# Performance work log

Hardware: AMD Instinct MI355X
Metric: run time of the kernel (lower is better)

## Reference

```python
import jax, jax.numpy as jnp
import numpy as np

FEAT_RES = 512
FEAT_DIM = 48
WIDTH = 128
IN_DIM = FEAT_DIM + 27 + 63  # 138
N_RAYS, N_SAMPLES = 4096, 128


def positional_encode(x, L):
    freqs = (2.0 ** jnp.arange(L)).astype(x.dtype)            # [L]
    xf = x[..., None, :] * freqs[:, None]                      # [..., L, 3]
    enc = jnp.concatenate([jnp.sin(xf), jnp.cos(xf)], axis=-1) # [..., L, 6]
    return jnp.concatenate([x, enc.reshape(x.shape[:-1] + (L * 6,))], axis=-1)


def grid_sample_bilinear(plane, gx, gy):
    # plane: [C, H, W]; gx, gy: [N, S] in [-1, 1]; align_corners=True, zeros padding
    H, W = plane.shape[-2], plane.shape[-1]
    ix = (gx + 1.0) * 0.5 * (W - 1)
    iy = (gy + 1.0) * 0.5 * (H - 1)
    x0 = jnp.floor(ix); y0 = jnp.floor(iy)
    x1 = x0 + 1.0;      y1 = y0 + 1.0
    wx1 = ix - x0; wx0 = 1.0 - wx1
    wy1 = iy - y0; wy0 = 1.0 - wy1

    def gather(xi, yi, w):
        valid = (xi >= 0) & (xi <= W - 1) & (yi >= 0) & (yi <= H - 1)
        xc = jnp.clip(xi, 0, W - 1).astype(jnp.int32)
        yc = jnp.clip(yi, 0, H - 1).astype(jnp.int32)
        v = plane[:, yc, xc]                                   # [C, N, S]
        return v * (w * valid.astype(w.dtype))[None]

    return (gather(x0, y0, wx0 * wy0) + gather(x1, y0, wx1 * wy0)
            + gather(x0, y1, wx0 * wy1) + gather(x1, y1, wx1 * wy1))


def setup_inputs() -> dict:
    key = jax.random.key(0)
    ks = jax.random.split(key, 12)
    x = jax.random.uniform(ks[0], (N_RAYS, N_SAMPLES, 3), jnp.float32, -3.0, 3.0)
    d = jax.random.normal(ks[1], (N_RAYS, 3), jnp.float32)
    d = d / jnp.linalg.norm(d, axis=-1, keepdims=True)
    feat = jax.random.normal(ks[2], (3, FEAT_DIM, FEAT_RES, FEAT_RES), jnp.float32)
    s = 0.05
    W0 = jax.random.normal(ks[3], (IN_DIM, WIDTH), jnp.float32) * s
    b0 = jnp.zeros((WIDTH,), jnp.float32)
    W1 = jax.random.normal(ks[4], (WIDTH, WIDTH), jnp.float32) * s
    b1 = jnp.zeros((WIDTH,), jnp.float32)
    W2 = jax.random.normal(ks[5], (WIDTH, WIDTH), jnp.float32) * s
    b2 = jnp.zeros((WIDTH,), jnp.float32)
    W3 = jax.random.normal(ks[6], (WIDTH, 4), jnp.float32) * s
    b3 = jnp.zeros((4,), jnp.float32)
    return {"x": x, "d": d, "feat": feat, "W0": W0, "b0": b0,
            "W1": W1, "b1": b1, "W2": W2, "b2": b2, "W3": W3, "b3": b3}


def reference(x, d, feat, W0, b0, W1, b1, W2, b2, W3, b3):
    x = x / 3.0                                                # [N, S, 3]
    f_xy = grid_sample_bilinear(feat[0], x[..., 0], x[..., 1])  # [C, N, S]
    f_yz = grid_sample_bilinear(feat[1], x[..., 1], x[..., 2])
    f_xz = grid_sample_bilinear(feat[2], x[..., 0], x[..., 2])
    f_sum = jnp.moveaxis(f_xy + f_yz + f_xz, 0, -1)            # [N, S, C]

    d_rep = jnp.broadcast_to(d[:, None, :], x.shape)           # [N, S, 3]
    h = jnp.concatenate([f_sum, positional_encode(d_rep, 4), positional_encode(x, 10)], axis=-1)

    h = jax.nn.relu(h @ W0 + b0)
    h = jax.nn.relu(h @ W1 + b1)
    h = jax.nn.relu(h @ W2 + b2)
    out = h @ W3 + b3                                          # [N, S, 4]
    return jnp.concatenate([out[..., :3], jax.nn.relu(out[..., 3:])], axis=-1)
```

## Files before the change

### kernel.cpp

```cpp
#include <hip/hip_runtime.h>
#include <hip/hip_bf16.h>
#include <cstdint>
#include <cstddef>

#define NPLANE 262144
#define HSTR 152
#define WS_FEAT_BYTE 131072
#define PW_LAYER 18432

typedef unsigned int uint;
typedef __attribute__((ext_vector_type(16))) float f32x16;
typedef __attribute__((ext_vector_type(8))) short short8;

__device__ __forceinline__ float blo(uint u){ union{uint i; float f;} v; v.i = u<<16; return v.f; }
__device__ __forceinline__ float bhi(uint u){ union{uint i; float f;} v; v.i = u & 0xffff0000u; return v.f; }
__device__ __forceinline__ unsigned short bf16u(float f){
    __hip_bfloat16 h = __float2bfloat16(f);
    return *reinterpret_cast<unsigned short*>(&h);
}
__device__ __forceinline__ f32x16 mfma_(short8 a, short8 b, f32x16 c){
    return __builtin_amdgcn_mfma_f32_32x32x16_bf16(a, b, c, 0,0,0);
}

__global__ __launch_bounds__(256) void prep_weights(const float* __restrict__ W0,
                                                    const float* __restrict__ W1,
                                                    const float* __restrict__ W2,
                                                    const float* __restrict__ b0,
                                                    const float* __restrict__ b1,
                                                    const float* __restrict__ b2,
                                                    unsigned short* __restrict__ ws){
    const int idx = blockIdx.x*256 + threadIdx.x;
    if (idx >= 3*PW_LAYER) return;
    const int L = idx / PW_LAYER, base = idx % PW_LAYER;
    const float* W = (L==0)? W0 : (L==1)? W1 : W2;
    const float* B = (L==0)? b0 : (L==1)? b1 : b2;
    const int KREAL = (L==0)? 138 : 128;
    const int e  = base & 7;
    const int l  = (base >> 3) & 63;
    const int fr = base >> 9;
    const int ks = fr >> 2, nt = fr & 3;
    const int k  = ks*16 + (l >> 5)*8 + e;
    const int n  = nt*32 + (l & 31);
    float v = 0.f;
    if (k < KREAL) v = W[k*128 + n];
    else if (k == KREAL) v = B[n];
    ws[idx] = bf16u(v);
}

__global__ __launch_bounds__(256) void transpose_feat_k(const float* __restrict__ feat,
                                                        unsigned short* __restrict__ featT){
    __shared__ unsigned short lb[256*50];
    const int tid = threadIdx.x;
    const int pos = blockIdx.x*256 + tid;
    const int p  = pos >> 18;
    const int yx = pos & (NPLANE-1);
    const float* src = feat + (size_t)p*48*NPLANE + yx;
    #pragma unroll 4
    for (int c = 0; c < 48; ++c){
        lb[tid*50 + c] = bf16u(src[(size_t)c*NPLANE]);
    }
    __syncthreads();
    uint4* dst = (uint4*)(featT + (size_t)blockIdx.x*(256*48));
    #pragma unroll
    for (int m = 0; m < 6; ++m){
        const int u4 = tid + m*256;
        const int byteoff = u4*16;
        const int smp = byteoff/96;
        const int off = (byteoff%96) >> 2;
        const uint* rw = (const uint*)(lb + smp*50);
        uint4 val; val.x = rw[off]; val.y = rw[off+1]; val.z = rw[off+2]; val.w = rw[off+3];
        dst[u4] = val;
    }
}

__device__ __forceinline__ void run_layer(unsigned short* H, const unsigned short* __restrict__ Wp,
                                          int lane, int ln31, int kg, const int* pr){
    const unsigned short* Hrow = H + ln31*HSTR;
    f32x16 acc[4];
    #pragma unroll
    for (int i=0;i<4;++i) acc[i] = (f32x16)0.f;
    #pragma unroll
    for (int h=0; h<2; ++h){
        short8 bf[10];
        #pragma unroll
        for (int i=0;i<10;++i){
            const int ks = i>>1, nt = 2*h + (i&1);
            bf[i] = *reinterpret_cast<const short8*>(Wp + (((ks*4+nt)*64 + lane) << 3));
        }
        #pragma unroll
        for (int ks=0; ks<5; ++ks){
            const short8 a = *reinterpret_cast<const short8*>(Hrow + ks*16 + kg*8);
            acc[2*h]   = mfma_(a, bf[2*ks],   acc[2*h]);
            acc[2*h+1] = mfma_(a, bf[2*ks+1], acc[2*h+1]);
        }
        #pragma unroll
        for (int i=0;i<8;++i){
            const int ks = 5 + (i>>1), nt = 2*h + (i&1);
            bf[i] = *reinterpret_cast<const short8*>(Wp + (((ks*4+nt)*64 + lane) << 3));
        }
        #pragma unroll
        for (int ks=5; ks<9; ++ks){
            const short8 a = *reinterpret_cast<const short8*>(Hrow + ks*16 + kg*8);
            acc[2*h]   = mfma_(a, bf[2*(ks-5)],   acc[2*h]);
            acc[2*h+1] = mfma_(a, bf[2*(ks-5)+1], acc[2*h+1]);
        }
    }
    #pragma unroll
    for (int nt=0;nt<4;++nt){
        #pragma unroll
        for (int r=0;r<16;++r){
            const int row = pr[r] >> 8;
            const int col = nt*32 + (pr[r] & 255);
            H[row*HSTR + col] = bf16u(fmaxf(acc[nt][r], 0.f));
        }
    }
}

__global__ __launch_bounds__(64, 4) void nerf_mfma(
    const float* __restrict__ x, const float* __restrict__ d,
    const unsigned short* __restrict__ featT,
    const unsigned short* __restrict__ wp0, const unsigned short* __restrict__ wp1,
    const unsigned short* __restrict__ wp2,
    const float* __restrict__ W3, const float* __restrict__ b3,
    float* __restrict__ out)
{
    __shared__ unsigned short H[32*HSTR];
    __shared__ uint sW3u[256];

    const int lane = threadIdx.x;
    const int ln31 = lane & 31, kg = lane >> 5;
    const int g0 = blockIdx.x * 32;

    short8 pa = {0,0,0,0,0,0,0,0}, pb = pa, qa = pa, qb = pa;
    if (kg == 0){
        pa[0] = (short)bf16u((float)ln31);
        pb[0] = (short)bf16u(1.0f);
        qa[0] = (short)bf16u(1.0f);
        qb[0] = (short)bf16u((float)ln31);
    }
    const f32x16 zz = (f32x16)0.f;
    const f32x16 D1 = __builtin_amdgcn_mfma_f32_32x32x16_bf16(pa, pb, zz, 0,0,0);
    const f32x16 D2 = __builtin_amdgcn_mfma_f32_32x32x16_bf16(qa, qb, zz, 0,0,0);
    int pr[16];
    #pragma unroll
    for (int r=0;r<16;++r) pr[r] = (((int)D1[r]) << 8) | (int)D2[r];

    #pragma unroll
    for (int j=0;j<4;++j){
        const int idx = lane*4 + j;
        const int k = idx >> 1, c = idx & 1;
        sW3u[idx] = ((uint)bf16u(W3[k*4 + 2*c])) | (((uint)bf16u(W3[k*4 + 2*c + 1])) << 16);
    }

    #pragma unroll
    for (int rr=0; rr<2; ++rr){
        int s32, m;
        if (rr == 0){ s32 = ln31; m = kg; }
        else {
            if (lane >= 32){
                const int k = lane - 32;
                if (k < 27){
                    const int ray = g0 >> 7;
                    float v;
                    if (k < 3) v = d[ray*3+k];
                    else {
                        const int l=(k-3)/6, r=(k-3)%6;
                        const float a = d[ray*3 + (r%3)] * (float)(1<<l);
                        v = (r<3)? sinf(a) : cosf(a);
                    }
                    const unsigned short bv = bf16u(v);
                    for (int s2=0;s2<32;++s2) H[s2*HSTR + 48 + k] = bv;
                }
                break;
            }
            s32 = lane; m = 2;
        }
        const int g = g0 + s32;
        const float xn = x[3*g+m]*(1.0f/3.0f);
        unsigned short* row = H + s32*HSTR;
        row[75+m] = bf16u(xn);
        float sv, cv;
        sincosf(xn, &sv, &cv);
        #pragma unroll
        for (int l=0;l<10;++l){
            row[78+l*6+m]   = bf16u(sv);
            row[78+l*6+3+m] = bf16u(cv);
            const float s2v = 2.0f*sv*cv;
            const float c2v = 1.0f - 2.0f*sv*sv;
            sv = s2v; cv = c2v;
        }
    }
    if (lane < 32){
        *(uint*)(H + lane*HSTR + 138)  = 0x00003f80u;
        *(uint2*)(H + lane*HSTR + 140) = make_uint2(0u, 0u);
    }

    #pragma unroll
    for (int rr=0; rr<3; ++rr){
        const int u = rr*64 + lane;
        const int s32 = u/6, ch = u - s32*6;
        const int g = g0 + s32;
        const float xn0 = x[3*g+0]*(1.0f/3.0f);
        const float xn1 = x[3*g+1]*(1.0f/3.0f);
        const float xn2 = x[3*g+2]*(1.0f/3.0f);
        const int c0 = ch*8;
        float acc[8];
        #pragma unroll
        for (int q=0;q<8;++q) acc[q]=0.f;
        #pragma unroll
        for (int p=0;p<3;++p){
            const float gx = (p==1)? xn1 : xn0;
            const float gy = (p==0)? xn1 : xn2;
            const float ix = ((gx+1.0f)*0.5f)*511.0f;
            const float iy = ((gy+1.0f)*0.5f)*511.0f;
            const float fx0 = floorf(ix), fy0 = floorf(iy);
            const float wx1 = ix - fx0, wy1 = iy - fy0;
            const float wx0 = 1.0f-wx1, wy0 = 1.0f-wy1;
            const int x0i = (int)fx0, y0i = (int)fy0;
            const int x0c = min(max(x0i,0),511),   x1c = min(max(x0i+1,0),511);
            const int y0c = min(max(y0i,0),511),   y1c = min(max(y0i+1,0),511);
            const uint r0 = (uint)(p*NPLANE + y0c*512);
            const uint r1 = (uint)(p*NPLANE + y1c*512);
            const uint  av[4] = {(r0+x0c)*48u, (r0+x1c)*48u, (r1+x0c)*48u, (r1+x1c)*48u};
            const float wv[4] = {wx0*wy0, wx1*wy0, wx0*wy1, wx1*wy1};
            #pragma unroll
            for (int cr=0;cr<4;++cr){
                const uint4 uv = *(const uint4*)(featT + av[cr] + c0);
                const float w = wv[cr];
                acc[0]+=w*blo(uv.x); acc[1]+=w*bhi(uv.x);
                acc[2]+=w*blo(uv.y); acc[3]+=w*bhi(uv.y);
                acc[4]+=w*blo(uv.z); acc[5]+=w*bhi(uv.z);
                acc[6]+=w*blo(uv.w); acc[7]+=w*bhi(uv.w);
            }
        }
        union { unsigned short us[8]; uint4 v; } pk;
        #pragma unroll
        for (int q=0;q<8;++q) pk.us[q] = bf16u(acc[q]);
        *(uint4*)(H + s32*HSTR + c0) = pk.v;
    }

    run_layer(H, wp0, lane, ln31, kg, pr);
    if (lane < 32) *(uint4*)(H + lane*HSTR + 128) = make_uint4(0x00003f80u,0u,0u,0u);
    else           *(uint4*)(H + ln31*HSTR + 136) = make_uint4(0u,0u,0u,0u);
    run_layer(H, wp1, lane, ln31, kg, pr);
    run_layer(H, wp2, lane, ln31, kg, pr);

    {
        const int s32 = lane >> 1, cp = lane & 1;
        const unsigned short* hrow = H + s32*HSTR;
        const float2 b3v = *(const float2*)(b3 + 2*cp);
        float a0 = b3v.x, a1 = b3v.y;
        #pragma unroll
        for (int q=0;q<16;++q){
            const uint4 u = *(const uint4*)(hrow + q*8);
            const int k = q*8;
            float h; uint wp_;
            h = blo(u.x); wp_ = sW3u[(k+0)*2+cp]; a0 += h*blo(wp_); a1 += h*bhi(wp_);
            h = bhi(u.x); wp_ = sW3u[(k+1)*2+cp]; a0 += h*blo(wp_); a1 += h*bhi(wp_);
            h = blo(u.y); wp_ = sW3u[(k+2)*2+cp]; a0 += h*blo(wp_); a1 += h*bhi(wp_);
            h = bhi(u.y); wp_ = sW3u[(k+3)*2+cp]; a0 += h*blo(wp_); a1 += h*bhi(wp_);
            h = blo(u.z); wp_ = sW3u[(k+4)*2+cp]; a0 += h*blo(wp_); a1 += h*bhi(wp_);
            h = bhi(u.z); wp_ = sW3u[(k+5)*2+cp]; a0 += h*blo(wp_); a1 += h*bhi(wp_);
            h = blo(u.w); wp_ = sW3u[(k+6)*2+cp]; a0 += h*blo(wp_); a1 += h*bhi(wp_);
            h = bhi(u.w); wp_ = sW3u[(k+7)*2+cp]; a0 += h*blo(wp_); a1 += h*bhi(wp_);
        }
        if (cp == 1) a1 = fmaxf(a1, 0.f);
        float2 o; o.x = a0; o.y = a1;
        *(float2*)(out + (size_t)(g0+s32)*4 + 2*cp) = o;
    }
}

#define STR 148
#define SBLK 64
template<int K4, int KTAIL>
__device__ __forceinline__ void mlp_layer_fb(float (*Hs)[STR], const float* __restrict__ W,
                                             const float* __restrict__ B, int tid){
    const int tx = tid & 31, ty = tid >> 5;
    const int s0 = ty*8, j0 = tx*4;
    float acc[8][4];
    #pragma unroll
    for (int i=0;i<8;++i){ acc[i][0]=0.f; acc[i][1]=0.f; acc[i][2]=0.f; acc[i][3]=0.f; }
    for (int kk = 0; kk < K4; ++kk){
        const int k = kk*4;
        const float4 wa = *(const float4*)(W + (size_t)(k+0)*128 + j0);
        const float4 wb = *(const float4*)(W + (size_t)(k+1)*128 + j0);
        const float4 wc = *(const float4*)(W + (size_t)(k+2)*128 + j0);
        const float4 wd = *(const float4*)(W + (size_t)(k+3)*128 + j0);
        #pragma unroll
        for (int i=0;i<8;++i){
            const float4 h = *(const float4*)&Hs[s0+i][k];
            acc[i][0] += h.x*wa.x + h.y*wb.x + h.z*wc.x + h.w*wd.x;
            acc[i][1] += h.x*wa.y + h.y*wb.y + h.z*wc.y + h.w*wd.y;
            acc[i][2] += h.x*wa.z + h.y*wb.z + h.z*wc.z + h.w*wd.z;
            acc[i][3] += h.x*wa.w + h.y*wb.w + h.z*wc.w + h.w*wd.w;
        }
    }
    #pragma unroll
    for (int t=0;t<KTAIL;++t){
        const int k = K4*4+t;
        const float4 wa = *(const float4*)(W + (size_t)k*128 + j0);
        #pragma unroll
        for (int i=0;i<8;++i){
            const float h = Hs[s0+i][k];
            acc[i][0] += h*wa.x; acc[i][1] += h*wa.y; acc[i][2] += h*wa.z; acc[i][3] += h*wa.w;
        }
    }
    const float4 bb = *(const float4*)(B + j0);
    __syncthreads();
    #pragma unroll
    for (int i=0;i<8;++i){
        float4 o;
        o.x = fmaxf(acc[i][0]+bb.x, 0.f);
        o.y = fmaxf(acc[i][1]+bb.y, 0.f);
        o.z = fmaxf(acc[i][2]+bb.z, 0.f);
        o.w = fmaxf(acc[i][3]+bb.w, 0.f);
        *(float4*)&Hs[s0+i][j0] = o;
    }
    __syncthreads();
}

__global__ __launch_bounds__(256) void nerf_fused_fb(
    const float* __restrict__ x, const float* __restrict__ d,
    const float* __restrict__ feat,
    const float* __restrict__ W0, const float* __restrict__ b0,
    const float* __restrict__ W1, const float* __restrict__ b1,
    const float* __restrict__ W2, const float* __restrict__ b2,
    const float* __restrict__ W3, const float* __restrict__ b3,
    float* __restrict__ out)
{
    __shared__ float Hs[SBLK][STR];
    __shared__ uint4  sA[3][SBLK];
    __shared__ float4 sW[3][SBLK];

    const int tid = threadIdx.x;
    const int g0 = blockIdx.x * SBLK;

    if (tid < 192){
        const int s = tid & 63, p = tid >> 6;
        const int g = g0 + s;
        const float xn0 = x[3*g+0]/3.0f, xn1 = x[3*g+1]/3.0f, xn2 = x[3*g+2]/3.0f;
        const float gx = (p==1)? xn1 : xn0;
        const float gy = (p==0)? xn1 : xn2;
        const float ix = ((gx+1.0f)*0.5f)*511.0f;
        const float iy = ((gy+1.0f)*0.5f)*511.0f;
        const float fx0 = floorf(ix), fy0 = floorf(iy);
        const float wx1 = ix - fx0, wy1 = iy - fy0;
        const float wx0 = 1.0f-wx1, wy0 = 1.0f-wy1;
        const int x0i = (int)fx0, y0i = (int)fy0;
        const int x0c = min(max(x0i,0),511),   x1c = min(max(x0i+1,0),511);
        const int y0c = min(max(y0i,0),511),   y1c = min(max(y0i+1,0),511);
        const uint bp = (uint)p*48u*NPLANE;
        sA[p][s] = make_uint4(bp + y0c*512 + x0c, bp + y0c*512 + x1c,
                              bp + y1c*512 + x0c, bp + y1c*512 + x1c);
        sW[p][s] = make_float4(wx0*wy0, wx1*wy0, wx0*wy1, wx1*wy1);
    }
    if (tid < 64){
        const int s = tid, g = g0 + s;
        float xn[3];
        xn[0]=x[3*g+0]/3.0f; xn[1]=x[3*g+1]/3.0f; xn[2]=x[3*g+2]/3.0f;
        Hs[s][75]=xn[0]; Hs[s][76]=xn[1]; Hs[s][77]=xn[2];
        float f = 1.0f;
        for (int l=0;l<10;++l){
            #pragma unroll
            for (int m=0;m<3;++m){
                const float a = xn[m]*f;
                Hs[s][78+l*6+m]   = sinf(a);
                Hs[s][78+l*6+3+m] = cosf(a);
            }
            f *= 2.0f;
        }
    } else if (tid < 91){
        const int k = tid-64;
        const int ray = g0 >> 7;
        float v;
        if (k < 3) v = d[ray*3+k];
        else {
            const int l=(k-3)/6, r=(k-3)%6;
            const float a = d[ray*3 + (r%3)] * (float)(1<<l);
            v = (r<3)? sinf(a) : cosf(a);
        }
        for (int s2=0;s2<64;++s2) Hs[s2][48+k]=v;
    }
    __syncthreads();

    for (int it = tid; it < 384; it += 256){
        const int s = it & 63;
        const int c0 = (it >> 6)*8;
        float acc[8];
        #pragma unroll
        for (int q=0;q<8;++q) acc[q]=0.f;
        #pragma unroll
        for (int p=0;p<3;++p){
            const uint4  aa = sA[p][s];
            const float4 ww = sW[p][s];
            const uint  av[4] = {aa.x,aa.y,aa.z,aa.w};
            const float wv[4] = {ww.x,ww.y,ww.z,ww.w};
            #pragma unroll
            for (int cr=0;cr<4;++cr){
                const float w = wv[cr];
                const float* bsrc = feat + av[cr] + (size_t)c0*NPLANE;
                #pragma unroll
                for (int q=0;q<8;++q) acc[q] += w*bsrc[(size_t)q*NPLANE];
            }
        }
        *(float4*)&Hs[s][c0]   = make_float4(acc[0],acc[1],acc[2],acc[3]);
        *(float4*)&Hs[s][c0+4] = make_float4(acc[4],acc[5],acc[6],acc[7]);
    }
    __syncthreads();

    mlp_layer_fb<34,2>(Hs, W0, b0, tid);
    mlp_layer_fb<32,0>(Hs, W1, b1, tid);
    mlp_layer_fb<32,0>(Hs, W2, b2, tid);

    {
        const int s = tid>>2, j = tid&3;
        float acc = 0.f;
        for (int kk=0; kk<32; ++kk){
            const float4 h = *(const float4*)&Hs[s][kk*4];
            const int k = kk*4;
            acc += h.x*W3[(k+0)*4+j] + h.y*W3[(k+1)*4+j]
                 + h.z*W3[(k+2)*4+j] + h.w*W3[(k+3)*4+j];
        }
        acc += b3[j];
        if (j==3) acc = fmaxf(acc, 0.f);
        out[(size_t)blockIdx.x*256 + tid] = acc;
    }
}

extern "C" void kernel_launch(void* const* d_in, const int* in_sizes, int n_in,
                              void* d_out, int out_size, void* d_ws, size_t ws_size,
                              hipStream_t stream){
    (void)in_sizes; (void)n_in; (void)out_size;
    const float* x    = (const float*)d_in[0];
    const float* ddir = (const float*)d_in[1];
    const float* feat = (const float*)d_in[2];
    const float* W0 = (const float*)d_in[3];  const float* b0 = (const float*)d_in[4];
    const float* W1 = (const float*)d_in[5];  const float* b1 = (const float*)d_in[6];
    const float* W2 = (const float*)d_in[7];  const float* b2 = (const float*)d_in[8];
    const float* W3 = (const float*)d_in[9];  const float* b3 = (const float*)d_in[10];
    float* out = (float*)d_out;

    const size_t needAll = (size_t)WS_FEAT_BYTE + (size_t)3*NPLANE*48*2;
    if (ws_size >= needAll){
        unsigned short* wsu   = (unsigned short*)d_ws;
        unsigned short* featT = (unsigned short*)((char*)d_ws + WS_FEAT_BYTE);
        prep_weights<<<216, 256, 0, stream>>>(W0, W1, W2, b0, b1, b2, wsu);
        transpose_feat_k<<<3072, 256, 0, stream>>>(feat, featT);
        nerf_mfma<<<16384, 64, 0, stream>>>(x, ddir, featT,
                                            wsu, wsu + PW_LAYER, wsu + 2*PW_LAYER,
                                            W3, b3, out);
    } else {
        nerf_fused_fb<<<8192, 256, 0, stream>>>(x, ddir, feat,
                                                W0,b0,W1,b1,W2,b2,W3,b3, out);
    }
}
```

Measured before the change: 271.9 us.

## Sort samples by Morton cell to improve feature-plane gather locality

Adds a histogram, scan and scatter pass that buckets the 524288 sample points by a 32^3 Morton-coded spatial cell, storing each point with its original index. The main MLP kernel then reads samples in sorted order, with block indices interleaved across eight groups, and writes outputs back to the original index. Direction encoding is now computed per sample instead of per ray, because a block may contain samples from many rays. The aim is to cut scattered feature-plane fetches by making spatially nearby samples share cache lines, at the cost of three extra kernels with atomics, a single-block scan, and more per-sample sincos work.

```diff
diff --git a/kernel.cpp b/kernel.cpp
--- a/kernel.cpp
+++ b/kernel.cpp
@@ -5,8 +5,16 @@
 
 #define NPLANE 262144
 #define HSTR 152
-#define WS_FEAT_BYTE 131072
 #define PW_LAYER 18432
+#define NCELL 32768
+#define NSAMP 524288
+
+#define WS_FEAT_OFF 131072
+#define FEAT_BYTES  75497472
+#define WS_CNT_OFF  (WS_FEAT_OFF + FEAT_BYTES)
+#define WS_OFFS_OFF (WS_CNT_OFF + 131072)
+#define WS_XS_OFF   (WS_OFFS_OFF + 131072)
+#define WS_END      (WS_XS_OFF + (size_t)NSAMP*16)
 
 typedef unsigned int uint;
 typedef __attribute__((ext_vector_type(16))) float f32x16;
@@ -20,6 +28,55 @@
 }
 __device__ __forceinline__ f32x16 mfma_(short8 a, short8 b, f32x16 c){
     return __builtin_amdgcn_mfma_f32_32x32x16_bf16(a, b, c, 0,0,0);
+}
+
+__device__ __forceinline__ uint part3(uint v){
+    v &= 0x3ff;
+    v = (v | (v<<16)) & 0x030000FFu;
+    v = (v | (v<<8))  & 0x0300F00Fu;
+    v = (v | (v<<4))  & 0x030C30C3u;
+    v = (v | (v<<2))  & 0x09249249u;
+    return v;
+}
+__device__ __forceinline__ uint cellkey(float x0, float x1, float x2){
+    const float s = 1.0f/3.0f;
+    const int cx = min(max((int)((x0*s+1.0f)*16.0f),0),31);
+    const int cy = min(max((int)((x1*s+1.0f)*16.0f),0),31);
+    const int cz = min(max((int)((x2*s+1.0f)*16.0f),0),31);
+    return part3((uint)cx) | (part3((uint)cy)<<1) | (part3((uint)cz)<<2);
+}
+
+__global__ __launch_bounds__(256) void hist_k(const float* __restrict__ x, uint* __restrict__ counts){
+    const int i = blockIdx.x*256 + threadIdx.x;
+    if (i >= NSAMP) return;
+    atomicAdd(&counts[cellkey(x[3*i], x[3*i+1], x[3*i+2])], 1u);
+}
+
+__global__ __launch_bounds__(1024) void scan_k(const uint* __restrict__ counts, uint* __restrict__ offs){
+    __shared__ uint ps[1024];
+    const int t = threadIdx.x;
+    uint loc[32]; uint s = 0;
+    #pragma unroll
+    for (int i=0;i<32;++i){ loc[i] = counts[t*32+i]; s += loc[i]; }
+    ps[t] = s; __syncthreads();
+    for (int off=1; off<1024; off<<=1){
+        uint v = (t>=off) ? ps[t-off] : 0u;
+        __syncthreads();
+        ps[t] += v;
+        __syncthreads();
+    }
+    uint base = ps[t] - s;
+    #pragma unroll
+    for (int i=0;i<32;++i){ offs[t*32+i] = base; base += loc[i]; }
+}
+
+__global__ __launch_bounds__(256) void scatter_k(const float* __restrict__ x, uint* __restrict__ offs,
+                                                 float4* __restrict__ xs){
+    const int i = blockIdx.x*256 + threadIdx.x;
+    if (i >= NSAMP) return;
+    const float x0 = x[3*i], x1 = x[3*i+1], x2 = x[3*i+2];
+    const uint pos = atomicAdd(&offs[cellkey(x0,x1,x2)], 1u);
+    xs[pos] = make_float4(x0, x1, x2, __int_as_float(i));
 }
 
 __global__ __launch_bounds__(256) void prep_weights(const float* __restrict__ W0,
@@ -116,20 +173,24 @@
     }
 }
 
+template<int SORTED>
 __global__ __launch_bounds__(64, 4) void nerf_mfma(
     const float* __restrict__ x, const float* __restrict__ d,
     const unsigned short* __restrict__ featT,
     const unsigned short* __restrict__ wp0, const unsigned short* __restrict__ wp1,
     const unsigned short* __restrict__ wp2,
     const float* __restrict__ W3, const float* __restrict__ b3,
-    float* __restrict__ out)
+    const float4* __restrict__ xs, float* __restrict__ out)
 {
     __shared__ unsigned short H[32*HSTR];
     __shared__ uint sW3u[256];
+    __shared__ float4 sX[32];
 
     const int lane = threadIdx.x;
     const int ln31 = lane & 31, kg = lane >> 5;
-    const int g0 = blockIdx.x * 32;
+    int base;
+    if (SORTED) base = (((int)blockIdx.x & 7)*2048 + ((int)blockIdx.x >> 3))*32;
+    else        base = (int)blockIdx.x*32;
 
     short8 pa = {0,0,0,0,0,0,0,0}, pb = pa, qa = pa, qb = pa;
     if (kg == 0){
@@ -145,6 +206,14 @@
     #pragma unroll
     for (int r=0;r<16;++r) pr[r] = (((int)D1[r]) << 8) | (int)D2[r];
 
+    if (lane < 32){
+        if (SORTED) sX[lane] = xs[base + lane];
+        else {
+            const int g = base + lane;
+            sX[lane] = make_float4(x[3*g], x[3*g+1], x[3*g+2], __int_as_float(g));
+        }
+    }
+
     #pragma unroll
     for (int j=0;j<4;++j){
         const int idx = lane*4 + j;
@@ -154,29 +223,11 @@
 
     #pragma unroll
     for (int rr=0; rr<2; ++rr){
-        int s32, m;
-        if (rr == 0){ s32 = ln31; m = kg; }
-        else {
-            if (lane >= 32){
-                const int k = lane - 32;
-                if (k < 27){
-                    const int ray = g0 >> 7;
-                    float v;
-                    if (k < 3) v = d[ray*3+k];
-                    else {
-                        const int l=(k-3)/6, r=(k-3)%6;
-                        const float a = d[ray*3 + (r%3)] * (float)(1<<l);
-                        v = (r<3)? sinf(a) : cosf(a);
-                    }
-                    const unsigned short bv = bf16u(v);
-                    for (int s2=0;s2<32;++s2) H[s2*HSTR + 48 + k] = bv;
-                }
-                break;
-            }
-            s32 = lane; m = 2;
-        }
-        const int g = g0 + s32;
-        const float xn = x[3*g+m]*(1.0f/3.0f);
+        if (rr == 1 && lane >= 32) break;
+        const int s32 = rr ? lane : ln31;
+        const int m   = rr ? 2 : kg;
+        const float4 xr = sX[s32];
+        const float xn = ((m==0)? xr.x : (m==1)? xr.y : xr.z) * (1.0f/3.0f);
         unsigned short* row = H + s32*HSTR;
         row[75+m] = bf16u(xn);
         float sv, cv;
@@ -190,6 +241,27 @@
             sv = s2v; cv = c2v;
         }
     }
+
+    {
+        const int s32 = lane >> 1, half = lane & 1;
+        const int sid = __float_as_int(sX[s32].w);
+        const int ray = sid >> 7;
+        const float dv0 = d[ray*3], dv1 = d[ray*3+1], dv2 = d[ray*3+2];
+        unsigned short* row = H + s32*HSTR;
+        if (half == 0){
+            row[48]=bf16u(dv0); row[49]=bf16u(dv1); row[50]=bf16u(dv2);
+        }
+        #pragma unroll
+        for (int li=0; li<2; ++li){
+            const int l = half*2 + li;
+            const float sc = (float)(1<<l);
+            float sv, cv;
+            sincosf(dv0*sc, &sv, &cv); row[51+l*6+0]=bf16u(sv); row[54+l*6+0]=bf16u(cv);
+            sincosf(dv1*sc, &sv, &cv); row[51+l*6+1]=bf16u(sv); row[54+l*6+1]=bf16u(cv);
+            sincosf(dv2*sc, &sv, &cv); row[51+l*6+2]=bf16u(sv); row[54+l*6+2]=bf16u(cv);
+        }
+    }
+
     if (lane < 32){
         *(uint*)(H + lane*HSTR + 138)  = 0x00003f80u;
         *(uint2*)(H + lane*HSTR + 140) = make_uint2(0u, 0u);
@@ -199,10 +271,10 @@
     for (int rr=0; rr<3; ++rr){
         const int u = rr*64 + lane;
         const int s32 = u/6, ch = u - s32*6;
-        const int g = g0 + s32;
-        const float xn0 = x[3*g+0]*(1.0f/3.0f);
-        const float xn1 = x[3*g+1]*(1.0f/3.0f);
-        const float xn2 = x[3*g+2]*(1.0f/3.0f);
+        const float4 xr = sX[s32];
+        const float xn0 = xr.x*(1.0f/3.0f);
+        const float xn1 = xr.y*(1.0f/3.0f);
+        const float xn2 = xr.z*(1.0f/3.0f);
         const int c0 = ch*8;
         float acc[8];
         #pragma unroll
@@ -248,6 +320,7 @@
     {
         const int s32 = lane >> 1, cp = lane & 1;
         const unsigned short* hrow = H + s32*HSTR;
+        const int sid = __float_as_int(sX[s32].w);
         const float2 b3v = *(const float2*)(b3 + 2*cp);
         float a0 = b3v.x, a1 = b3v.y;
         #pragma unroll
@@ -266,7 +339,7 @@
         }
         if (cp == 1) a1 = fmaxf(a1, 0.f);
         float2 o; o.x = a0; o.y = a1;
-        *(float2*)(out + (size_t)(g0+s32)*4 + 2*cp) = o;
+        *(float2*)(out + (size_t)sid*4 + 2*cp) = o;
     }
 }
 
@@ -440,15 +513,29 @@
     const float* W3 = (const float*)d_in[9];  const float* b3 = (const float*)d_in[10];
     float* out = (float*)d_out;
 
-    const size_t needAll = (size_t)WS_FEAT_BYTE + (size_t)3*NPLANE*48*2;
-    if (ws_size >= needAll){
-        unsigned short* wsu   = (unsigned short*)d_ws;
-        unsigned short* featT = (unsigned short*)((char*)d_ws + WS_FEAT_BYTE);
+    char* wsb = (char*)d_ws;
+    unsigned short* wsu   = (unsigned short*)wsb;
+    unsigned short* featT = (unsigned short*)(wsb + WS_FEAT_OFF);
+
+    if (ws_size >= WS_END){
+        uint*   counts = (uint*)(wsb + WS_CNT_OFF);
+        uint*   offs   = (uint*)(wsb + WS_OFFS_OFF);
+        float4* xsrec  = (float4*)(wsb + WS_XS_OFF);
+        hipMemsetAsync(counts, 0, NCELL*sizeof(uint), stream);
         prep_weights<<<216, 256, 0, stream>>>(W0, W1, W2, b0, b1, b2, wsu);
         transpose_feat_k<<<3072, 256, 0, stream>>>(feat, featT);
-        nerf_mfma<<<16384, 64, 0, stream>>>(x, ddir, featT,
-                                            wsu, wsu + PW_LAYER, wsu + 2*PW_LAYER,
-                                            W3, b3, out);
+        hist_k<<<2048, 256, 0, stream>>>(x, counts);
+        scan_k<<<1, 1024, 0, stream>>>(counts, offs);
+        scatter_k<<<2048, 256, 0, stream>>>(x, offs, xsrec);
+        nerf_mfma<1><<<16384, 64, 0, stream>>>(x, ddir, featT,
+                                               wsu, wsu + PW_LAYER, wsu + 2*PW_LAYER,
+                                               W3, b3, xsrec, out);
+    } else if (ws_size >= WS_CNT_OFF){
+        prep_weights<<<216, 256, 0, stream>>>(W0, W1, W2, b0, b1, b2, wsu);
+        transpose_feat_k<<<3072, 256, 0, stream>>>(feat, featT);
+        nerf_mfma<0><<<16384, 64, 0, stream>>>(x, ddir, featT,
+                                               wsu, wsu + PW_LAYER, wsu + 2*PW_LAYER,
+                                               W3, b3, nullptr, out);
     } else {
         nerf_fused_fb<<<8192, 256, 0, stream>>>(x, ddir, feat,
                                                 W0,b0,W1,b1,W2,b2,W3,b3, out);
```

Measured after the change: 276.1 us. No clear change (+1.6%).
